# Performance work log

Hardware: AMD Instinct MI355X
Metric: run time of the kernel (lower is better)

## Reference

```python
import jax, jax.numpy as jnp
import numpy as np

D_MODEL = 1024
DK = 64
H = D_MODEL // DK
EPS = 1e-5


def setup_inputs() -> dict:
    key = jax.random.key(0)
    ks = jax.random.split(key, 8)
    B, M = 4, 2048
    s = 1.0 / np.sqrt(D_MODEL)
    return {
        "inp": jax.random.normal(ks[0], (B, M, D_MODEL), dtype=jnp.float32),
        "Wq": jax.random.normal(ks[1], (D_MODEL, D_MODEL), dtype=jnp.float32) * s,
        "bq": jnp.zeros((D_MODEL,), dtype=jnp.float32),
        "Wk": jax.random.normal(ks[2], (D_MODEL, D_MODEL), dtype=jnp.float32) * s,
        "bk": jnp.zeros((D_MODEL,), dtype=jnp.float32),
        "Wv": jax.random.normal(ks[3], (D_MODEL, D_MODEL), dtype=jnp.float32) * s,
        "bv": jnp.zeros((D_MODEL,), dtype=jnp.float32),
        "gamma": jnp.ones((D_MODEL,), dtype=jnp.float32),
        "beta": jnp.zeros((D_MODEL,), dtype=jnp.float32),
    }


def reference(inp, Wq, bq, Wk, bk, Wv, bv, gamma, beta):
    B, M, _ = inp.shape
    # LayerNorm over last dim
    mu = jnp.mean(inp, axis=-1, keepdims=True)
    var = jnp.mean(jnp.square(inp - mu), axis=-1, keepdims=True)
    out = (inp - mu) * jax.lax.rsqrt(var + EPS) * gamma + beta
    # QKV projections (x @ W + b)
    Q = (out @ Wq + bq).reshape(B, M, DK, H)
    K = (out @ Wk + bk).reshape(B, M, DK, H)
    V = (out @ Wv + bv).reshape(B, M, DK, H)
    # per-position attention over the dk axis, contracting h
    scores = jnp.einsum("bmih,bmjh->bmij", Q, K) / np.sqrt(DK)  # [B,M,dk,dk]
    att = jax.nn.softmax(scores, axis=-1)
    res = jnp.einsum("bmij,bmjh->bmih", att, V).reshape(B, M, D_MODEL)
    # dropout is identity at eval; positionals add in original is dead code
    return inp + res
```

## Files before the change

### kernel.cpp

```cpp
#include <hip/hip_runtime.h>
#include <hip/hip_bf16.h>

#define D_MODEL 1024
#define NQKV 3072

typedef __attribute__((ext_vector_type(8))) short bf16x8;
typedef __attribute__((ext_vector_type(4))) float f32x4;
typedef __attribute__((ext_vector_type(16))) float f32x16;
typedef __attribute__((ext_vector_type(8))) unsigned short u16x8;

static __device__ __forceinline__ unsigned short f2bf(float f){
  unsigned int x = __float_as_uint(f);
  x += 0x7fff + ((x >> 16) & 1);
  return (unsigned short)(x >> 16);
}
static __device__ __forceinline__ float bf2f(unsigned short u){
  return __uint_as_float(((unsigned int)u) << 16);
}

__global__ __launch_bounds__(256) void ln_kernel(const float* __restrict__ inp,
    const float* __restrict__ gamma, const float* __restrict__ beta,
    unsigned short* __restrict__ X){
  const int row = blockIdx.x;
  const int t = threadIdx.x;
  const float4* ip = (const float4*)(inp + (size_t)row * D_MODEL);
  float4 v = ip[t];
  float s1 = v.x + v.y + v.z + v.w;
  float s2 = v.x*v.x + v.y*v.y + v.z*v.z + v.w*v.w;
#pragma unroll
  for (int off = 32; off >= 1; off >>= 1){
    s1 += __shfl_down(s1, off);
    s2 += __shfl_down(s2, off);
  }
  __shared__ float red[8];
  const int wave = t >> 6, lane = t & 63;
  if (lane == 0){ red[wave] = s1; red[4 + wave] = s2; }
  __syncthreads();
  s1 = red[0] + red[1] + red[2] + red[3];
  s2 = red[4] + red[5] + red[6] + red[7];
  const float mu   = s1 * (1.0f / D_MODEL);
  const float var  = s2 * (1.0f / D_MODEL) - mu * mu;
  const float rstd = rsqrtf(var + 1e-5f);
  float4 g = ((const float4*)gamma)[t];
  float4 b = ((const float4*)beta)[t];
  ushort4 o;
  o.x = f2bf((v.x - mu) * rstd * g.x + b.x);
  o.y = f2bf((v.y - mu) * rstd * g.y + b.y);
  o.z = f2bf((v.z - mu) * rstd * g.z + b.z);
  o.w = f2bf((v.w - mu) * rstd * g.w + b.w);
  ((ushort4*)(X + (size_t)row * D_MODEL))[t] = o;
}

__global__ __launch_bounds__(256) void wtrans_kernel(const float* __restrict__ Wq,
    const float* __restrict__ Wk, const float* __restrict__ Wv,
    unsigned short* __restrict__ Wt){
  __shared__ float tile[32][33];
  const float* W = (blockIdx.z == 0) ? Wq : ((blockIdx.z == 1) ? Wk : Wv);
  const int k0 = blockIdx.x * 32, n0 = blockIdx.y * 32;
  const int r = threadIdx.x >> 5, c = threadIdx.x & 31;
#pragma unroll
  for (int i = 0; i < 4; i++)
    tile[r + i*8][c] = W[(size_t)(k0 + r + i*8) * D_MODEL + n0 + c];
  __syncthreads();
  unsigned short* dst = Wt + (size_t)(blockIdx.z * D_MODEL + n0) * D_MODEL + k0;
#pragma unroll
  for (int i = 0; i < 4; i++){
    int rr = r + i*8;
    dst[(size_t)rr * D_MODEL + c] = f2bf(tile[c][rr]);
  }
}

__global__ void biascat_kernel(const float* __restrict__ bq, const float* __restrict__ bk,
                               const float* __restrict__ bv, float* __restrict__ bc){
  int i = blockIdx.x * 256 + threadIdx.x;
  float v = (i < 1024) ? bq[i] : (i < 2048) ? bk[i - 1024] : bv[i - 2048];
  bc[i] = v;
}


#define GLL(src, dst) __builtin_amdgcn_global_load_lds( \
    (const __attribute__((address_space(1))) void*)(src), \
    (__attribute__((address_space(3))) void*)(dst), 16, 0, 0)

#define STAGE(tsrc, bi) do { \
  const char* _sa = Ag + (size_t)r0*2048 + (size_t)(tsrc)*128 + co; \
  char* _da = ldsS + (size_t)(bi)*49152 + tid*16; \
  GLL(_sa, _da); GLL(_sa + 131072, _da + 8192); \
  const char* _sb = Bg + (size_t)r0*2048 + (size_t)(tsrc)*128 + co; \
  char* _db = ldsS + (size_t)(bi)*49152 + 16384 + tid*16; \
  GLL(_sb, _db); GLL(_sb + 131072, _db + 8192); \
  GLL(_sb + 262144, _db + 16384); GLL(_sb + 393216, _db + 24576); \
} while(0)

#define BODY(bi) do { \
  const char* Ab = ldsS + (size_t)(bi)*49152 + (wr*64 + lr)*128; \
  const char* Bb = ldsS + (size_t)(bi)*49152 + 16384 + (wc*64 + lr)*128; \
  bf16x8 Ar[4][2], Br[4][2]; \
  _Pragma("unroll") \
  for (int m = 0; m < 4; m++){ \
    Ar[m][0] = *(const bf16x8*)(Ab + m*2048 + colb0); \
    Ar[m][1] = *(const bf16x8*)(Ab + m*2048 + colb1); \
  } \
  _Pragma("unroll") \
  for (int n = 0; n < 4; n++){ \
    Br[n][0] = *(const bf16x8*)(Bb + n*2048 + colb0); \
    Br[n][1] = *(const bf16x8*)(Bb + n*2048 + colb1); \
  } \
  _Pragma("unroll") \
  for (int m = 0; m < 4; m++) \
    _Pragma("unroll") \
    for (int n = 0; n < 4; n++){ \
      acc[m][n] = __builtin_amdgcn_mfma_f32_16x16x32_bf16(Ar[m][0], Br[n][0], acc[m][n], 0, 0, 0); \
      acc[m][n] = __builtin_amdgcn_mfma_f32_16x16x32_bf16(Ar[m][1], Br[n][1], acc[m][n], 0, 0, 0); \
    } \
} while(0)

#define BARRIER __builtin_amdgcn_s_barrier()
#define SCHEDB  __builtin_amdgcn_sched_barrier(0)
#define VMCNT6  asm volatile("s_waitcnt vmcnt(6)" ::: "memory")
#define VMCNT0  asm volatile("s_waitcnt vmcnt(0)" ::: "memory")

__global__ __launch_bounds__(512, 2) void gemm128x256_kernel(const unsigned short* __restrict__ A,
    const unsigned short* __restrict__ Bt, const float* __restrict__ bias,
    unsigned short* __restrict__ C){
  __shared__ __align__(16) char ldsS[3 * 49152];
  const int tid = threadIdx.x;
  const int wave = tid >> 6, lane = tid & 63;
  const int wr = wave >> 2, wc = wave & 3;
  const int lr = lane & 15;
  const int colb0 = ((lane >> 4) * 16) ^ ((lane & 7) << 4);
  const int colb1 = (64 + (lane >> 4) * 16) ^ ((lane & 7) << 4);

  const int b = blockIdx.x;
  const int swz = (b & 7) * 96 + (b >> 3);
  const int m0 = (swz & 63) * 128;
  const int n0 = (swz >> 6) * 256;

  const int r0 = tid >> 3;
  const size_t co = (size_t)(((tid & 7) * 16) ^ ((r0 & 7) << 4));
  const char* Ag = (const char*)(A + (size_t)m0 * 1024);
  const char* Bg = (const char*)(Bt + (size_t)n0 * 1024);

  f32x4 acc[4][4] = {};

  STAGE(0, 0);
  STAGE(1, 1);

  for (int t = 0; t < 15; ++t){
    SCHEDB; VMCNT6; BARRIER; SCHEDB;
    if (t <= 13) STAGE(t + 2, (t + 2) % 3);
    BODY(t % 3);
  }
  SCHEDB; VMCNT0; BARRIER; SCHEDB;
  BODY(0);

  const int gm = m0 + wr*64;
  const int gn = n0 + wc*64;
  const int rr0 = (lane >> 4) * 4;
#pragma unroll
  for (int nf = 0; nf < 4; nf++){
    const int gcol = gn + nf*16 + lr;
    const float bb = bias[gcol];
#pragma unroll
    for (int mf = 0; mf < 4; mf++){
      const int grow = gm + mf*16 + rr0;
#pragma unroll
      for (int r = 0; r < 4; r++)
        C[(size_t)(grow + r) * NQKV + gcol] = f2bf(acc[mf][nf][r] + bb);
    }
  }
}

__global__ __launch_bounds__(256) void attn_kernel(const unsigned short* __restrict__ qkv,
    const float* __restrict__ inp, float* __restrict__ out){
  __shared__ unsigned short P[4][64 * 64];
  const int wave = threadIdx.x >> 6, lane = threadIdx.x & 63;
  const int token = blockIdx.x * 4 + wave;
  const unsigned short* row = qkv + (size_t)token * NQKV;
  const int l31 = lane & 31, hi = lane >> 5;
  const int l15 = lane & 15, qg = lane >> 4;
  char* pbase = (char*)&P[wave][0];

  bf16x8 kf[2], qf[2];
#pragma unroll
  for (int mt = 0; mt < 2; mt++)
    kf[mt] = *(const bf16x8*)(row + 1024 + (mt*32 + l31)*16 + hi*8);
#pragma unroll
  for (int nt = 0; nt < 2; nt++)
    qf[nt] = *(const bf16x8*)(row + (nt*32 + l31)*16 + hi*8);

  bf16x8 vf[2];
#pragma unroll
  for (int kc = 0; kc < 2; kc++)
#pragma unroll
    for (int e = 0; e < 8; e++)
      vf[kc][e] = (short)row[2048 + (kc*32 + qg*8 + e)*16 + l15];

  f32x16 s[2][2] = {};
#pragma unroll
  for (int mt = 0; mt < 2; mt++)
#pragma unroll
    for (int nt = 0; nt < 2; nt++)
      s[mt][nt] = __builtin_amdgcn_mfma_f32_32x32x16_bf16(kf[mt], qf[nt], s[mt][nt], 0, 0, 0);

#pragma unroll
  for (int ti = 0; ti < 2; ti++){
    float m = s[0][ti][0];
#pragma unroll
    for (int mt = 0; mt < 2; mt++)
#pragma unroll
      for (int r = 0; r < 16; r++) m = fmaxf(m, s[mt][ti][r]);
    m = fmaxf(m, __shfl_xor(m, 32));
    float sum = 0.0f;
#pragma unroll
    for (int mt = 0; mt < 2; mt++)
#pragma unroll
      for (int r = 0; r < 16; r++){
        float p = exp2f((s[mt][ti][r] - m) * 0.1803368801f);
        s[mt][ti][r] = p;
        sum += p;
      }
    sum += __shfl_xor(sum, 32);
    const float invs = 1.0f / sum;
    const int i = ti*32 + l31;
    const int sw = (i & 7) << 4;
#pragma unroll
    for (int mt = 0; mt < 2; mt++)
#pragma unroll
      for (int g = 0; g < 4; g++){
        ushort4 pk;
        pk.x = f2bf(s[mt][ti][4*g + 0] * invs);
        pk.y = f2bf(s[mt][ti][4*g + 1] * invs);
        pk.z = f2bf(s[mt][ti][4*g + 2] * invs);
        pk.w = f2bf(s[mt][ti][4*g + 3] * invs);
        const int jbyte = mt*64 + g*16 + hi*8;
        *(ushort4*)(pbase + ((i*128 + jbyte) ^ sw)) = pk;
      }
  }
  __syncthreads();

  f32x4 o[4] = {};
#pragma unroll
  for (int nt = 0; nt < 4; nt++){
    const int n = nt*16 + l15;
    const int swr = (n & 7) << 4;
#pragma unroll
    for (int kc = 0; kc < 2; kc++){
      bf16x8 pb = *(const bf16x8*)(pbase + ((n*128 + kc*64 + qg*16) ^ swr));
      o[nt] = __builtin_amdgcn_mfma_f32_16x16x32_bf16(vf[kc], pb, o[nt], 0, 0, 0);
    }
  }

  const size_t base = (size_t)token * D_MODEL;
#pragma unroll
  for (int nt = 0; nt < 4; nt++){
    const int i = nt*16 + l15;
    const float4 iv = *(const float4*)(inp + base + i*16 + qg*4);
    float4 ov;
    ov.x = iv.x + o[nt][0];
    ov.y = iv.y + o[nt][1];
    ov.z = iv.z + o[nt][2];
    ov.w = iv.w + o[nt][3];
    *(float4*)(out + base + i*16 + qg*4) = ov;
  }
}

extern "C" void kernel_launch(void* const* d_in, const int* in_sizes, int n_in,
                              void* d_out, int out_size, void* d_ws, size_t ws_size,
                              hipStream_t stream) {
  const float* inp   = (const float*)d_in[0];
  const float* Wq    = (const float*)d_in[1];
  const float* bq    = (const float*)d_in[2];
  const float* Wk    = (const float*)d_in[3];
  const float* bk    = (const float*)d_in[4];
  const float* Wv    = (const float*)d_in[5];
  const float* bv    = (const float*)d_in[6];
  const float* gamma = (const float*)d_in[7];
  const float* beta  = (const float*)d_in[8];
  float* out = (float*)d_out;

  char* ws = (char*)d_ws;
  unsigned short* Xln  = (unsigned short*)ws;
  unsigned short* Wt   = (unsigned short*)(ws + 16777216);
  float*          bc   = (float*)(ws + 23068672);
  unsigned short* QKV  = (unsigned short*)(ws + 23080960);

  ln_kernel<<<8192, 256, 0, stream>>>(inp, gamma, beta, Xln);
  wtrans_kernel<<<dim3(32, 32, 3), 256, 0, stream>>>(Wq, Wk, Wv, Wt);
  biascat_kernel<<<12, 256, 0, stream>>>(bq, bk, bv, bc);
  gemm128x256_kernel<<<768, 512, 0, stream>>>(Xln, Wt, bc, QKV);
  attn_kernel<<<2048, 256, 0, stream>>>(QKV, inp, out);
}
```

Measured before the change: 100.9 us.

## Split K across wave groups in QKV GEMM with LDS reduction

Reorganizes the 8 waves of the 128x256 GEMM block from a 2x4 output grid into a 2x2 output grid with two K-halves per tile. Each wave now computes a 64x128 sub-tile over half of each 64-wide K slice. This improves register-level reuse: 4 A fragments and 8 B fragments feed 32 MFMAs, versus 16 fragments for 32 MFMAs before. The cost is doubled accumulator registers, an epilogue that reduces partial sums through LDS with extra barriers, and only half the waves doing the stores.

```diff
diff --git a/kernel.cpp b/kernel.cpp
--- a/kernel.cpp
+++ b/kernel.cpp
@@ -93,26 +93,18 @@
 } while(0)
 
 #define BODY(bi) do { \
-  const char* Ab = ldsS + (size_t)(bi)*49152 + (wr*64 + lr)*128; \
-  const char* Bb = ldsS + (size_t)(bi)*49152 + 16384 + (wc*64 + lr)*128; \
-  bf16x8 Ar[4][2], Br[4][2]; \
+  const char* Ab = ldsS + (size_t)(bi)*49152 + (wm*64 + lr)*128; \
+  const char* Bb = ldsS + (size_t)(bi)*49152 + 16384 + (wn*128 + lr)*128; \
+  bf16x8 Ar[4], Br[8]; \
   _Pragma("unroll") \
-  for (int m = 0; m < 4; m++){ \
-    Ar[m][0] = *(const bf16x8*)(Ab + m*2048 + colb0); \
-    Ar[m][1] = *(const bf16x8*)(Ab + m*2048 + colb1); \
-  } \
+  for (int m = 0; m < 4; m++) Ar[m] = *(const bf16x8*)(Ab + m*2048 + colbk); \
   _Pragma("unroll") \
-  for (int n = 0; n < 4; n++){ \
-    Br[n][0] = *(const bf16x8*)(Bb + n*2048 + colb0); \
-    Br[n][1] = *(const bf16x8*)(Bb + n*2048 + colb1); \
-  } \
+  for (int n = 0; n < 8; n++) Br[n] = *(const bf16x8*)(Bb + n*2048 + colbk); \
   _Pragma("unroll") \
   for (int m = 0; m < 4; m++) \
     _Pragma("unroll") \
-    for (int n = 0; n < 4; n++){ \
-      acc[m][n] = __builtin_amdgcn_mfma_f32_16x16x32_bf16(Ar[m][0], Br[n][0], acc[m][n], 0, 0, 0); \
-      acc[m][n] = __builtin_amdgcn_mfma_f32_16x16x32_bf16(Ar[m][1], Br[n][1], acc[m][n], 0, 0, 0); \
-    } \
+    for (int n = 0; n < 8; n++) \
+      acc[m][n] = __builtin_amdgcn_mfma_f32_16x16x32_bf16(Ar[m], Br[n], acc[m][n], 0, 0, 0); \
 } while(0)
 
 #define BARRIER __builtin_amdgcn_s_barrier()
@@ -126,10 +118,11 @@
   __shared__ __align__(16) char ldsS[3 * 49152];
   const int tid = threadIdx.x;
   const int wave = tid >> 6, lane = tid & 63;
-  const int wr = wave >> 2, wc = wave & 3;
+  const int kw = wave >> 2;
+  const int wm = (wave >> 1) & 1, wn = wave & 1;
   const int lr = lane & 15;
-  const int colb0 = ((lane >> 4) * 16) ^ ((lane & 7) << 4);
-  const int colb1 = (64 + (lane >> 4) * 16) ^ ((lane & 7) << 4);
+  const int x7 = (lane & 7) << 4;
+  const int colbk = (kw*64 + ((lane >> 4) * 16)) ^ x7;
 
   const int b = blockIdx.x;
   const int swz = (b & 7) * 96 + (b >> 3);
@@ -141,7 +134,7 @@
   const char* Ag = (const char*)(A + (size_t)m0 * 1024);
   const char* Bg = (const char*)(Bt + (size_t)n0 * 1024);
 
-  f32x4 acc[4][4] = {};
+  f32x4 acc[4][8] = {};
 
   STAGE(0, 0);
   STAGE(1, 1);
@@ -154,19 +147,48 @@
   SCHEDB; VMCNT0; BARRIER; SCHEDB;
   BODY(0);
 
-  const int gm = m0 + wr*64;
-  const int gn = n0 + wc*64;
-  const int rr0 = (lane >> 4) * 4;
-#pragma unroll
-  for (int nf = 0; nf < 4; nf++){
-    const int gcol = gn + nf*16 + lr;
-    const float bb = bias[gcol];
-#pragma unroll
-    for (int mf = 0; mf < 4; mf++){
-      const int grow = gm + mf*16 + rr0;
-#pragma unroll
-      for (int r = 0; r < 4; r++)
-        C[(size_t)(grow + r) * NQKV + gcol] = f2bf(acc[mf][nf][r] + bb);
+  const int pairSlot = wm*2 + wn;
+#pragma unroll
+  for (int rdx = 0; rdx < 2; ++rdx){
+    __syncthreads();
+    if (kw == 1){
+#pragma unroll
+      for (int i = 0; i < 2; ++i){
+        const int mf = rdx*2 + i;
+#pragma unroll
+        for (int nf = 0; nf < 8; ++nf)
+          *(f32x4*)(ldsS + pairSlot*16384 + (i*8 + nf)*1024 + lane*16) = acc[mf][nf];
+      }
+    }
+    __syncthreads();
+    if (kw == 0){
+#pragma unroll
+      for (int i = 0; i < 2; ++i){
+        const int mf = rdx*2 + i;
+#pragma unroll
+        for (int nf = 0; nf < 8; ++nf){
+          f32x4 p = *(const f32x4*)(ldsS + pairSlot*16384 + (i*8 + nf)*1024 + lane*16);
+          acc[mf][nf] += p;
+        }
+      }
+    }
+  }
+
+  if (kw == 0){
+    const int gm = m0 + wm*64;
+    const int gn = n0 + wn*128;
+    const int rr0 = (lane >> 4) * 4;
+#pragma unroll
+    for (int nf = 0; nf < 8; nf++){
+      const int gcol = gn + nf*16 + lr;
+      const float bb = bias[gcol];
+#pragma unroll
+      for (int mf = 0; mf < 4; mf++){
+        const int grow = gm + mf*16 + rr0;
+#pragma unroll
+        for (int r = 0; r < 4; r++)
+          C[(size_t)(grow + r) * NQKV + gcol] = f2bf(acc[mf][nf][r] + bb);
+      }
     }
   }
 }
```

After: 101.7 us. About the same (+0.8%).

## Shrink QKV GEMM tile to 128x128 with double buffering and 256 threads

Applied to the files above, without the earlier changes.

Replaces the 128x256 tile, 512-thread, triple-buffered GEMM with a 128x128 tile, 256-thread, double-buffered version launched on twice as many blocks. The LDS footprint drops from 144KB to 64KB per block, which may allow more resident blocks and better load balance across CUs. In exchange, operand reuse per tile is lower, and the loop now waits for all outstanding loads (vmcnt 0) before each step, so there is less latency hiding.

```diff
diff --git a/kernel.cpp b/kernel.cpp
--- a/kernel.cpp
+++ b/kernel.cpp
@@ -83,18 +83,19 @@
     (__attribute__((address_space(3))) void*)(dst), 16, 0, 0)
 
 #define STAGE(tsrc, bi) do { \
-  const char* _sa = Ag + (size_t)r0*2048 + (size_t)(tsrc)*128 + co; \
-  char* _da = ldsS + (size_t)(bi)*49152 + tid*16; \
-  GLL(_sa, _da); GLL(_sa + 131072, _da + 8192); \
-  const char* _sb = Bg + (size_t)r0*2048 + (size_t)(tsrc)*128 + co; \
-  char* _db = ldsS + (size_t)(bi)*49152 + 16384 + tid*16; \
-  GLL(_sb, _db); GLL(_sb + 131072, _db + 8192); \
-  GLL(_sb + 262144, _db + 16384); GLL(_sb + 393216, _db + 24576); \
+  _Pragma("unroll") \
+  for (int q = 0; q < 4; q++){ \
+    const int idx = q*256 + tid; \
+    const int row = idx >> 3; \
+    const size_t scol = (size_t)((tsrc)*128) + (((idx & 7)*16) ^ ((row & 7) << 4)); \
+    GLL(Ag + (size_t)row*2048 + scol, ldsS + (size_t)(bi)*32768 + idx*16); \
+    GLL(Bg + (size_t)row*2048 + scol, ldsS + (size_t)(bi)*32768 + 16384 + idx*16); \
+  } \
 } while(0)
 
 #define BODY(bi) do { \
-  const char* Ab = ldsS + (size_t)(bi)*49152 + (wr*64 + lr)*128; \
-  const char* Bb = ldsS + (size_t)(bi)*49152 + 16384 + (wc*64 + lr)*128; \
+  const char* Ab = ldsS + (size_t)(bi)*32768 + (wm*64 + lr)*128; \
+  const char* Bb = ldsS + (size_t)(bi)*32768 + 16384 + (wn*64 + lr)*128; \
   bf16x8 Ar[4][2], Br[4][2]; \
   _Pragma("unroll") \
   for (int m = 0; m < 4; m++){ \
@@ -117,45 +118,41 @@
 
 #define BARRIER __builtin_amdgcn_s_barrier()
 #define SCHEDB  __builtin_amdgcn_sched_barrier(0)
-#define VMCNT6  asm volatile("s_waitcnt vmcnt(6)" ::: "memory")
 #define VMCNT0  asm volatile("s_waitcnt vmcnt(0)" ::: "memory")
 
-__global__ __launch_bounds__(512, 2) void gemm128x256_kernel(const unsigned short* __restrict__ A,
+__global__ __launch_bounds__(256, 2) void gemm128_kernel(const unsigned short* __restrict__ A,
     const unsigned short* __restrict__ Bt, const float* __restrict__ bias,
     unsigned short* __restrict__ C){
-  __shared__ __align__(16) char ldsS[3 * 49152];
+  __shared__ __align__(16) char ldsS[2 * 32768];
   const int tid = threadIdx.x;
   const int wave = tid >> 6, lane = tid & 63;
-  const int wr = wave >> 2, wc = wave & 3;
+  const int wm = wave >> 1, wn = wave & 1;
   const int lr = lane & 15;
-  const int colb0 = ((lane >> 4) * 16) ^ ((lane & 7) << 4);
-  const int colb1 = (64 + (lane >> 4) * 16) ^ ((lane & 7) << 4);
+  const int x7 = (lane & 7) << 4;
+  const int colb0 = ((lane >> 4) * 16) ^ x7;
+  const int colb1 = (64 + (lane >> 4) * 16) ^ x7;
 
   const int b = blockIdx.x;
-  const int swz = (b & 7) * 96 + (b >> 3);
+  const int swz = (b & 7) * 192 + (b >> 3);
   const int m0 = (swz & 63) * 128;
-  const int n0 = (swz >> 6) * 256;
-
-  const int r0 = tid >> 3;
-  const size_t co = (size_t)(((tid & 7) * 16) ^ ((r0 & 7) << 4));
+  const int n0 = (swz >> 6) * 128;
+
   const char* Ag = (const char*)(A + (size_t)m0 * 1024);
   const char* Bg = (const char*)(Bt + (size_t)n0 * 1024);
 
   f32x4 acc[4][4] = {};
 
   STAGE(0, 0);
-  STAGE(1, 1);
-
-  for (int t = 0; t < 15; ++t){
-    SCHEDB; VMCNT6; BARRIER; SCHEDB;
-    if (t <= 13) STAGE(t + 2, (t + 2) % 3);
-    BODY(t % 3);
-  }
-  SCHEDB; VMCNT0; BARRIER; SCHEDB;
-  BODY(0);
-
-  const int gm = m0 + wr*64;
-  const int gn = n0 + wc*64;
+
+  int buf = 0;
+  for (int t = 0; t < 16; ++t, buf ^= 1){
+    SCHEDB; VMCNT0; BARRIER; SCHEDB;
+    if (t < 15) STAGE(t + 1, buf ^ 1);
+    BODY(buf);
+  }
+
+  const int gm = m0 + wm*64;
+  const int gn = n0 + wn*64;
   const int rr0 = (lane >> 4) * 4;
 #pragma unroll
   for (int nf = 0; nf < 4; nf++){
@@ -288,6 +285,6 @@
   ln_kernel<<<8192, 256, 0, stream>>>(inp, gamma, beta, Xln);
   wtrans_kernel<<<dim3(32, 32, 3), 256, 0, stream>>>(Wq, Wk, Wv, Wt);
   biascat_kernel<<<12, 256, 0, stream>>>(bq, bk, bv, bc);
-  gemm128x256_kernel<<<768, 512, 0, stream>>>(Xln, Wt, bc, QKV);
+  gemm128_kernel<<<1536, 256, 0, stream>>>(Xln, Wt, bc, QKV);
   attn_kernel<<<2048, 256, 0, stream>>>(QKV, inp, out);
 }
```

Measured after the change: 109.3 us. +8.3%, slower.
